# Kernel optimization log

Hardware: AMD Instinct MI355X
Metric: run time of the kernel (lower is better)

The kernel has to match this reference:

```python
import jax, jax.numpy as jnp
import numpy as np
import math

B, C, MAPS, HEADS, F, W = 2, 8, 4, 8, 256, 1024
HD = F // HEADS  # head dim = 32


def conv2d(x, w, b):
    # x [B,Ci,H,W], w [Co,Ci,3,3], SAME padding 1
    y = jax.lax.conv_general_dilated(x, w, (1, 1), [(1, 1), (1, 1)],
                                     dimension_numbers=('NCHW', 'OIHW', 'NCHW'))
    return y + b[None, :, None, None]


def mcl_feat(x, w):
    # MultichannelLinear feature transform: per-channel linear over feature dim
    # x [B,C,Fin,W], w [C,Fout,Fin] -> [B,C,Fout,W]
    return jnp.einsum('bcfw,cgf->bcgw', x, w)


def rope(x):
    # lucidrains-style rotary embedding over seq dim (-2); x [..., S, D]
    d = x.shape[-1]
    s = x.shape[-2]
    inv = 1.0 / (10000.0 ** (jnp.arange(0, d, 2, dtype=jnp.float32) / d))
    fr = jnp.arange(s, dtype=jnp.float32)[:, None] * inv[None, :]  # [S, D/2]
    cos = jnp.repeat(jnp.cos(fr), 2, axis=-1).astype(x.dtype)  # [S, D]
    sin = jnp.repeat(jnp.sin(fr), 2, axis=-1).astype(x.dtype)
    x2 = x.reshape(*x.shape[:-1], d // 2, 2)
    xr = jnp.stack((-x2[..., 1], x2[..., 0]), axis=-1).reshape(x.shape)
    return x * cos + xr * sin


def setup_inputs() -> dict:
    key = jax.random.key(0)
    ks = jax.random.split(key, 16)
    p = lambda k, shp, s=0.02: (jax.random.normal(k, shp, dtype=jnp.float32) * s)
    inp = {
        'x': jax.random.normal(ks[0], (B, C, F, W), dtype=jnp.float32),
        'prev_qk': jax.random.normal(ks[1], (B, MAPS, HEADS, W, W), dtype=jnp.float32),
        'wq_conv': p(ks[2], (MAPS, C, 3, 3)), 'bq_conv': jnp.zeros((MAPS,), jnp.float32),
        'wq_lin': p(ks[3], (MAPS, F, F)),
        'wk_conv': p(ks[4], (MAPS, C, 3, 3)), 'bk_conv': jnp.zeros((MAPS,), jnp.float32),
        'wk_lin': p(ks[5], (MAPS, F, F)),
        'wv_conv': p(ks[6], (MAPS, C, 3, 3)), 'bv_conv': jnp.zeros((MAPS,), jnp.float32),
        'wv_lin': p(ks[7], (MAPS, F, F)),
        'wo_pw': p(ks[8], (C + MAPS, F, F)),
        'wo_dw': p(ks[9], (C, C + MAPS)),
    }
    return inp


def reference(x, prev_qk, wq_conv, bq_conv, wq_lin, wk_conv, bk_conv, wk_lin,
              wv_conv, bv_conv, wv_lin, wo_pw, wo_dw):
    b, c, h, w = x.shape

    def proj(w_conv, b_conv, w_lin):
        y = mcl_feat(conv2d(x, w_conv, b_conv), w_lin)  # [B,M,F,W]
        # transpose(2,3) -> [B,M,W,F] -> split heads -> [B,M,Hd,W? ] permute
        y = y.transpose(0, 1, 3, 2).reshape(b, MAPS, w, HEADS, HD)
        return y.transpose(0, 1, 3, 2, 4)  # [B,M,Heads,W,HD]

    q = rope(proj(wq_conv, bq_conv, wq_lin))
    k = rope(proj(wk_conv, bk_conv, wk_lin))
    v = proj(wv_conv, bv_conv, wv_lin)

    # NOTE: scale is sqrt(h) = sqrt(feature/height dim), as in the original code
    qk = jnp.einsum('bmnqd,bmnkd->bmnqk', q, k) / math.sqrt(h)
    qk = qk + prev_qk
    a = jnp.einsum('bmnqk,bmnkd->bmnqd', jax.nn.softmax(qk, axis=-1), v)
    # [B,M,Heads,W,HD] -> [B,M,W,Heads*HD] -> [B,M,F,W]
    a = a.transpose(0, 1, 3, 2, 4).reshape(b, MAPS, w, -1).transpose(0, 1, 3, 2)

    cat = jnp.concatenate((x, a), axis=1)  # [B, C+M, F, W]
    out = jnp.einsum('bcfw,oc->bofw', mcl_feat(cat, wo_pw), wo_dw)  # o_proj
    return out, qk
```

## Files before the change

kernel.cpp:

```cpp
#include <hip/hip_runtime.h>
#include <hip/hip_bf16.h>
#include <stdint.h>


typedef __attribute__((ext_vector_type(8))) short s16x8;
typedef __attribute__((ext_vector_type(4))) float f32x4;

#define MFMA16(a, b, c) __builtin_amdgcn_mfma_f32_16x16x32_bf16((a), (b), (c), 0, 0, 0)

__device__ __forceinline__ short f2bf(float f) {
  unsigned u = __builtin_bit_cast(unsigned, f);
  u = (u + 0x7FFFu + ((u >> 16) & 1u)) >> 16;
  return (short)u;
}
__device__ __forceinline__ unsigned pack2(float a, float b) {
  return (unsigned)(unsigned short)f2bf(a) | ((unsigned)(unsigned short)f2bf(b) << 16);
}
__device__ __forceinline__ float bf2f(unsigned u) {
  return __builtin_bit_cast(float, u << 16);
}

__global__ __launch_bounds__(256) void k_prep(const float* wq, const float* wk,
                                              const float* wv, const float* wo,
                                              short* wlin, short* wob, float* ct, float* st) {
  int i = blockIdx.x * 256 + threadIdx.x;
  if (i < 262144) wlin[i] = f2bf(wq[i]);
  else if (i < 524288) wlin[i] = f2bf(wk[i - 262144]);
  else if (i < 786432) wlin[i] = f2bf(wv[i - 524288]);
  if (i < 786432) wob[i] = f2bf(wo[i]);
  if (i < 16384) {
    int w = i >> 4, j = i & 15;
    float inv = exp2f(-(float)j * (13.287712379549449f / 16.0f));
    float ang = (float)w * inv;
    ct[i] = cosf(ang);
    st[i] = sinf(ang);
  }
}

__device__ __forceinline__ void loadrow(float* r, const float* xc, int f, int w0) {
  if (f < 0 || f > 255) {
#pragma unroll
    for (int jj = 0; jj < 6; ++jj) r[jj] = 0.f;
    return;
  }
  const float* row = xc + f * 1024;
#pragma unroll
  for (int jj = 0; jj < 6; ++jj) {
    int wc = w0 - 1 + jj;
    r[jj] = (wc >= 0 && wc < 1024) ? row[wc] : 0.f;
  }
}

__global__ __launch_bounds__(256) void k_conv(const float* x, const float* wqc, const float* bq,
                                              const float* wkc, const float* bk,
                                              const float* wvc, const float* bv, short* y) {
  int blk = blockIdx.x;
  int m_ = blk >> 7;
  int b_ = (blk >> 6) & 1;
  int fs = blk & 63;
  int f0 = fs * 4;
  int w0 = threadIdx.x * 4;
  const float* xb = x + (size_t)b_ * 2097152;
  const float* wp_[3] = {wqc + m_ * 72, wkc + m_ * 72, wvc + m_ * 72};
  float bias_[3] = {bq[m_], bk[m_], bv[m_]};

  float acc[3][4][4];
#pragma unroll
  for (int p = 0; p < 3; ++p)
#pragma unroll
    for (int fi = 0; fi < 4; ++fi)
#pragma unroll
      for (int j = 0; j < 4; ++j) acc[p][fi][j] = bias_[p];

  for (int c = 0; c < 8; ++c) {
    const float* xc = xb + c * 262144;
    float w9[3][9];
#pragma unroll
    for (int p = 0; p < 3; ++p)
#pragma unroll
      for (int t = 0; t < 9; ++t) w9[p][t] = wp_[p][c * 9 + t];
    float rows[6][6];
#pragma unroll
    for (int ri = 0; ri < 6; ++ri) loadrow(rows[ri], xc, f0 - 1 + ri, w0);
#pragma unroll
    for (int fi = 0; fi < 4; ++fi) {
#pragma unroll
      for (int p = 0; p < 3; ++p) {
#pragma unroll
        for (int j = 0; j < 4; ++j) {
          float s = acc[p][fi][j];
          s += rows[fi][j] * w9[p][0] + rows[fi][j + 1] * w9[p][1] + rows[fi][j + 2] * w9[p][2];
          s += rows[fi + 1][j] * w9[p][3] + rows[fi + 1][j + 1] * w9[p][4] + rows[fi + 1][j + 2] * w9[p][5];
          s += rows[fi + 2][j] * w9[p][6] + rows[fi + 2][j + 1] * w9[p][7] + rows[fi + 2][j + 2] * w9[p][8];
          acc[p][fi][j] = s;
        }
      }
    }
  }
#pragma unroll
  for (int p = 0; p < 3; ++p) {
    int mat = p * 8 + b_ * 4 + m_;
    short* yp = y + (size_t)mat * 262144;
#pragma unroll
    for (int fi = 0; fi < 4; ++fi) {
      uint2 pk;
      pk.x = pack2(acc[p][fi][0], acc[p][fi][1]);
      pk.y = pack2(acc[p][fi][2], acc[p][fi][3]);
      *(uint2*)(yp + (f0 + fi) * 1024 + w0) = pk;
    }
  }
}

__global__ __launch_bounds__(256) void k_ty(const short* y, short* yT) {
  __shared__ short tile[64][66];
  int blk = blockIdx.x;
  int mat = blk >> 6;
  int t = blk & 63;
  int f0 = (t >> 4) * 64, w0 = (t & 15) * 64;
  int j = threadIdx.x & 63, i0 = threadIdx.x >> 6;
  const short* sp = y + (size_t)mat * 262144 + f0 * 1024 + w0;
#pragma unroll
  for (int k = 0; k < 16; ++k) {
    int i = i0 + k * 4;
    tile[j][i] = sp[i * 1024 + j];
  }
  __syncthreads();
  short* dp = yT + (size_t)mat * 262144 + w0 * 256 + f0;
#pragma unroll
  for (int k = 0; k < 16; ++k) {
    int i = i0 + k * 4;
    dp[i * 256 + j] = tile[i][j];
  }
}

__global__ __launch_bounds__(256) void k_tx(const float* x, short* xT) {
  __shared__ short tile[64][66];
  int blk = blockIdx.x;
  int mat = blk >> 6;
  int t = blk & 63;
  int f0 = (t >> 4) * 64, w0 = (t & 15) * 64;
  int j = threadIdx.x & 63, i0 = threadIdx.x >> 6;
  const float* sp = x + (size_t)mat * 262144 + f0 * 1024 + w0;
#pragma unroll
  for (int k = 0; k < 16; ++k) {
    int i = i0 + k * 4;
    tile[j][i] = f2bf(sp[i * 1024 + j]);
  }
  __syncthreads();
  short* dp = xT + (size_t)mat * 262144 + w0 * 256 + f0;
#pragma unroll
  for (int k = 0; k < 16; ++k) {
    int i = i0 + k * 4;
    dp[i * 256 + j] = tile[i][j];
  }
}

__global__ __launch_bounds__(256) void k_qkv(const short* wlin, const short* yT,
                                             const float* ct, const float* st,
                                             short* qws, short* kws, short* vws) {
  int blk = blockIdx.x;
  int pbm = blk >> 4, wt = blk & 15;
  int p = pbm >> 3, bm = pbm & 7;
  int m_ = bm & 3;
  int tid = threadIdx.x, wv = tid >> 6, l = tid & 63, lr = l & 15, lg = l >> 4;
  const short* wl = wlin + (p * 4 + m_) * 65536;
  const short* yp = yT + (size_t)pbm * 262144;
  int w0 = wt * 64;
  int G0 = wv * 64;
  f32x4 acc[4][4];
#pragma unroll
  for (int i = 0; i < 4; ++i)
#pragma unroll
    for (int j = 0; j < 4; ++j) acc[i][j] = (f32x4){0.f, 0.f, 0.f, 0.f};

  if (p < 2) {
    for (int kc = 0; kc < 256; kc += 32) {
      s16x8 A[4], Bf[4];
#pragma unroll
      for (int gs = 0; gs < 4; ++gs)
        A[gs] = *(const s16x8*)(wl + (G0 + gs * 16 + lr) * 256 + kc + lg * 8);
#pragma unroll
      for (int s = 0; s < 4; ++s)
        Bf[s] = *(const s16x8*)(yp + (w0 + s * 16 + lr) * 256 + kc + lg * 8);
#pragma unroll
      for (int gs = 0; gs < 4; ++gs)
#pragma unroll
        for (int s = 0; s < 4; ++s) acc[gs][s] = MFMA16(A[gs], Bf[s], acc[gs][s]);
    }
    short* dst = (p == 0) ? qws : kws;
    float scale = (p == 0) ? 0.0625f : 1.0f;
#pragma unroll
    for (int gs = 0; gs < 4; ++gs) {
      int g0v = G0 + gs * 16 + lg * 4;
      int h = g0v >> 5, d0 = g0v & 31;
      int i0 = d0 >> 1;
#pragma unroll
      for (int s = 0; s < 4; ++s) {
        int w = w0 + s * 16 + lr;
        float c0 = ct[w * 16 + i0], sn0 = st[w * 16 + i0];
        float c1 = ct[w * 16 + i0 + 1], sn1 = st[w * 16 + i0 + 1];
        f32x4 v = acc[gs][s];
        float e0 = (v[0] * c0 - v[1] * sn0) * scale;
        float e1 = (v[1] * c0 + v[0] * sn0) * scale;
        float e2 = (v[2] * c1 - v[3] * sn1) * scale;
        float e3 = (v[3] * c1 + v[2] * sn1) * scale;
        uint2 pk;
        pk.x = pack2(e0, e1);
        pk.y = pack2(e2, e3);
        *(uint2*)(dst + (((size_t)bm * 8 + h) * 1024 + w) * 32 + d0) = pk;
      }
    }
  } else {
    for (int kc = 0; kc < 256; kc += 32) {
      s16x8 A[4], Bf[4];
#pragma unroll
      for (int s = 0; s < 4; ++s)
        A[s] = *(const s16x8*)(yp + (w0 + s * 16 + lr) * 256 + kc + lg * 8);
#pragma unroll
      for (int gs = 0; gs < 4; ++gs)
        Bf[gs] = *(const s16x8*)(wl + (G0 + gs * 16 + lr) * 256 + kc + lg * 8);
#pragma unroll
      for (int s = 0; s < 4; ++s)
#pragma unroll
        for (int gs = 0; gs < 4; ++gs) acc[s][gs] = MFMA16(A[s], Bf[gs], acc[s][gs]);
    }
#pragma unroll
    for (int s = 0; s < 4; ++s) {
      int wb = w0 + s * 16 + lg * 4;
#pragma unroll
      for (int gs = 0; gs < 4; ++gs) {
        int g = G0 + gs * 16 + lr;
        f32x4 v = acc[s][gs];
        uint2 pk;
        pk.x = pack2(v[0], v[1]);
        pk.y = pack2(v[2], v[3]);
        *(uint2*)(vws + ((size_t)bm * 256 + g) * 1024 + wb) = pk;
      }
    }
  }
}

__global__ __launch_bounds__(256, 1) void k_attn(const short* qws, const short* kws,
                                                 const short* vws, const float* prev,
                                                 float* qko, short* aT) {
  __shared__ char smem[131072];
  int blk = blockIdx.x;
  int bmh = blk >> 4;
  int qg = blk & 15;
  int h = bmh & 7, bm = bmh >> 3;
  int tid = threadIdx.x;
  int wv = tid >> 6, l = tid & 63, lr = l & 15, lg = l >> 4;
  int q0 = qg * 64 + wv * 16;
  const short* qp = qws + (size_t)bmh * 32768;
  const short* kp = kws + (size_t)bmh * 32768;
  const short* vp = vws + ((size_t)bm * 256 + h * 32) * 1024;
  const float* pvb = prev + (size_t)bmh * 1048576 + (size_t)q0 * 1024;
  float* qob = qko + (size_t)bmh * 1048576 + (size_t)q0 * 1024;
  char* Sb = smem + wv * 32768;

  s16x8 qf = *(const s16x8*)(qp + (q0 + lr) * 32 + lg * 8);
  const f32x4 z4 = {0.f, 0.f, 0.f, 0.f};

#pragma unroll
  for (int w = 0; w < 16; ++w) {
    int k0 = w * 64;
    s16x8 kf[4];
#pragma unroll
    for (int s = 0; s < 4; ++s)
      kf[s] = *(const s16x8*)(kp + (k0 + s * 16 + lr) * 32 + lg * 8);
#pragma unroll
    for (int s = 0; s < 4; ++s) {
      f32x4 sx = MFMA16(kf[s], qf, z4);
      uint2 pk;
      pk.x = pack2(sx[0], sx[1]);
      pk.y = pack2(sx[2], sx[3]);
      int kb = (k0 + s * 16 + lg * 4) * 2;
      *(uint2*)(Sb + lr * 2048 + (kb ^ ((lr & 7) << 4))) = pk;
    }
  }

  float rs[16];
  f32x4 pf[3][4];
#pragma unroll
  for (int qt = 0; qt < 4; ++qt) pf[0][qt] = *(const f32x4*)(pvb + 0 * 1024 + qt * 256 + l * 4);
#pragma unroll
  for (int qt = 0; qt < 4; ++qt) pf[1][qt] = *(const f32x4*)(pvb + 1 * 1024 + qt * 256 + l * 4);
#pragma unroll
  for (int qt = 0; qt < 4; ++qt) pf[2][qt] = *(const f32x4*)(pvb + 2 * 1024 + qt * 256 + l * 4);

#pragma unroll
  for (int r = 0; r < 16; ++r) {
    float sum = 0.f;
#pragma unroll
    for (int qt = 0; qt < 4; ++qt) {
      int sb = (qt * 512 + l * 8) ^ ((r & 7) << 4);
      uint2 su = *(const uint2*)(Sb + r * 2048 + sb);
      f32x4 sv = {bf2f(su.x & 0xffffu), bf2f(su.x >> 16),
                  bf2f(su.y & 0xffffu), bf2f(su.y >> 16)};
      f32x4 v = sv + pf[r % 3][qt];
      *(f32x4*)(qob + (size_t)r * 1024 + qt * 256 + l * 4) = v;
      float e0 = __expf(v[0]), e1 = __expf(v[1]);
      float e2 = __expf(v[2]), e3 = __expf(v[3]);
      sum += (e0 + e1) + (e2 + e3);
      uint2 pk;
      pk.x = pack2(e0, e1);
      pk.y = pack2(e2, e3);
      *(uint2*)(Sb + r * 2048 + sb) = pk;
    }
    if (r + 3 < 16) {
#pragma unroll
      for (int qt = 0; qt < 4; ++qt)
        pf[r % 3][qt] = *(const f32x4*)(pvb + (size_t)(r + 3) * 1024 + qt * 256 + l * 4);
    }
    rs[r] = sum;
  }
#pragma unroll
  for (int r = 0; r < 16; ++r) {
    float s = rs[r];
    s += __shfl_xor(s, 1);
    s += __shfl_xor(s, 2);
    s += __shfl_xor(s, 4);
    s += __shfl_xor(s, 8);
    s += __shfl_xor(s, 16);
    s += __shfl_xor(s, 32);
    rs[r] = s;
  }

  f32x4 o0 = {0.f, 0.f, 0.f, 0.f}, o1 = {0.f, 0.f, 0.f, 0.f};
#pragma unroll
  for (int w = 0; w < 16; ++w) {
    int k0 = w * 64;
#pragma unroll
    for (int kc = 0; kc < 2; ++kc) {
      int kb = (k0 + kc * 32 + lg * 8) * 2;
      s16x8 pa = *(const s16x8*)(Sb + lr * 2048 + (kb ^ ((lr & 7) << 4)));
      s16x8 vf0 = *(const s16x8*)(vp + lr * 1024 + k0 + kc * 32 + lg * 8);
      o0 = MFMA16(pa, vf0, o0);
      s16x8 vf1 = *(const s16x8*)(vp + (16 + lr) * 1024 + k0 + kc * 32 + lg * 8);
      o1 = MFMA16(pa, vf1, o1);
    }
  }
#pragma unroll
  for (int j = 0; j < 4; ++j) {
    float s = (lg == 0) ? rs[j] : (lg == 1) ? rs[4 + j] : (lg == 2) ? rs[8 + j] : rs[12 + j];
    float inv = 1.0f / s;
    o0[j] *= inv;
    o1[j] *= inv;
  }
  short* ap = aT + (size_t)bm * 262144;
#pragma unroll
  for (int r = 0; r < 4; ++r) {
    int row = q0 + lg * 4 + r;
    ap[row * 256 + h * 32 + lr] = f2bf(o0[r]);
    ap[row * 256 + h * 32 + 16 + lr] = f2bf(o1[r]);
  }
}

__global__ __launch_bounds__(256) void k_zproj(const short* wopw, const short* xT,
                                               const short* aT, short* z) {
  int blk = blockIdx.x;
  int bc = blk >> 4, wt = blk & 15;
  int b_ = bc / 12, c_ = bc % 12;
  const short* src = (c_ < 8) ? (xT + ((size_t)b_ * 8 + c_) * 262144)
                              : (aT + ((size_t)b_ * 4 + (c_ - 8)) * 262144);
  const short* wl = wopw + c_ * 65536;
  int tid = threadIdx.x, wv = tid >> 6, l = tid & 63, lr = l & 15, lg = l >> 4;
  int w0 = wt * 64, G0 = wv * 64;
  f32x4 acc[4][4];
#pragma unroll
  for (int i = 0; i < 4; ++i)
#pragma unroll
    for (int j = 0; j < 4; ++j) acc[i][j] = (f32x4){0.f, 0.f, 0.f, 0.f};
  for (int kc = 0; kc < 256; kc += 32) {
    s16x8 A[4], Bf[4];
#pragma unroll
    for (int s = 0; s < 4; ++s)
      A[s] = *(const s16x8*)(src + (w0 + s * 16 + lr) * 256 + kc + lg * 8);
#pragma unroll
    for (int gs = 0; gs < 4; ++gs)
      Bf[gs] = *(const s16x8*)(wl + (G0 + gs * 16 + lr) * 256 + kc + lg * 8);
#pragma unroll
    for (int s = 0; s < 4; ++s)
#pragma unroll
      for (int gs = 0; gs < 4; ++gs) acc[s][gs] = MFMA16(A[s], Bf[gs], acc[s][gs]);
  }
  short* zp = z + (size_t)bc * 262144;
#pragma unroll
  for (int s = 0; s < 4; ++s) {
    int wb = w0 + s * 16 + lg * 4;
#pragma unroll
    for (int gs = 0; gs < 4; ++gs) {
      int g = G0 + gs * 16 + lr;
      f32x4 v = acc[s][gs];
      uint2 pk;
      pk.x = pack2(v[0], v[1]);
      pk.y = pack2(v[2], v[3]);
      *(uint2*)(zp + g * 1024 + wb) = pk;
    }
  }
}

__global__ __launch_bounds__(256) void k_dw(const short* z, const float* dw, float* out0) {
  __shared__ float wdw[96];
  if (threadIdx.x < 96) wdw[threadIdx.x] = dw[threadIdx.x];
  __syncthreads();
  int id = blockIdx.x * 256 + threadIdx.x;
  int w4 = id & 255, g = (id >> 8) & 255, b_ = id >> 16;
  const short* zb = z + ((size_t)b_ * 12) * 262144 + g * 1024 + w4 * 4;
  float zv[12][4];
#pragma unroll
  for (int c = 0; c < 12; ++c) {
    uint2 u = *(const uint2*)(zb + (size_t)c * 262144);
    zv[c][0] = bf2f(u.x & 0xffffu);
    zv[c][1] = bf2f(u.x >> 16);
    zv[c][2] = bf2f(u.y & 0xffffu);
    zv[c][3] = bf2f(u.y >> 16);
  }
  float* ob = out0 + ((size_t)b_ * 8) * 262144 + g * 1024 + w4 * 4;
#pragma unroll
  for (int o = 0; o < 8; ++o) {
    f32x4 s = {0.f, 0.f, 0.f, 0.f};
#pragma unroll
    for (int c = 0; c < 12; ++c) {
      float wc = wdw[o * 12 + c];
      s[0] += wc * zv[c][0];
      s[1] += wc * zv[c][1];
      s[2] += wc * zv[c][2];
      s[3] += wc * zv[c][3];
    }
    __builtin_nontemporal_store(s, (f32x4*)(ob + (size_t)o * 262144));
  }
}

extern "C" void kernel_launch(void* const* d_in, const int* in_sizes, int n_in,
                              void* d_out, int out_size, void* d_ws, size_t ws_size,
                              hipStream_t stream) {
  const float* x = (const float*)d_in[0];
  const float* prevqk = (const float*)d_in[1];
  const float* wq_conv = (const float*)d_in[2];
  const float* bq = (const float*)d_in[3];
  const float* wq_lin = (const float*)d_in[4];
  const float* wk_conv = (const float*)d_in[5];
  const float* bk = (const float*)d_in[6];
  const float* wk_lin = (const float*)d_in[7];
  const float* wv_conv = (const float*)d_in[8];
  const float* bv = (const float*)d_in[9];
  const float* wv_lin = (const float*)d_in[10];
  const float* wo_pw = (const float*)d_in[11];
  const float* wo_dw = (const float*)d_in[12];

  float* out0 = (float*)d_out;
  float* qkout = out0 + 4194304;

  char* ws = (char*)d_ws;
  short* wlin_b = (short*)ws;
  short* wopw_b = wlin_b + 786432;
  float* ct = (float*)(ws + 3145728);
  float* st = ct + 16384;
  short* y_b = (short*)(ws + 3276800);
  short* yT_b = y_b + 6291456;
  short* q_b = yT_b + 6291456;
  short* k_b = q_b + 2097152;
  short* v_b = k_b + 2097152;
  short* xT_b = v_b + 2097152;
  short* aT_b = xT_b + 4194304;
  short* z_b = (short*)(ws + 53608448);

  k_prep<<<3072, 256, 0, stream>>>(wq_lin, wk_lin, wv_lin, wo_pw, wlin_b, wopw_b, ct, st);
  k_conv<<<512, 256, 0, stream>>>(x, wq_conv, bq, wk_conv, bk, wv_conv, bv, y_b);
  k_ty<<<1536, 256, 0, stream>>>(y_b, yT_b);
  k_tx<<<1024, 256, 0, stream>>>(x, xT_b);
  k_qkv<<<384, 256, 0, stream>>>(wlin_b, yT_b, ct, st, q_b, k_b, v_b);
  k_attn<<<1024, 256, 0, stream>>>(q_b, k_b, v_b, prevqk, qkout, aT_b);
  k_zproj<<<384, 256, 0, stream>>>(wopw_b, xT_b, aT_b, z_b);
  k_dw<<<512, 256, 0, stream>>>(z_b, wo_dw, out0);
}
```

Before: 253.2 us.

## Merge prep, conv and x-transpose kernels; batch prev_qk loads with nontemporal stores

Three independent preprocessing kernels (weight bf16 conversion plus rope tables, the 3x3 conv, and the x transpose) are folded into one launch that dispatches on block index, removing two launches and letting their blocks run concurrently. In the attention softmax stage, prev_qk loads are restructured into double-buffered groups of four rows. The qk output is written with nontemporal stores before the exp pass. This raises register pressure in the attention kernel and puts heterogeneous blocks in one grid with a shared-memory tile that only some blocks use.

```diff
diff --git a/kernel.cpp b/kernel.cpp
--- a/kernel.cpp
+++ b/kernel.cpp
@@ -20,23 +20,6 @@
   return __builtin_bit_cast(float, u << 16);
 }
 
-__global__ __launch_bounds__(256) void k_prep(const float* wq, const float* wk,
-                                              const float* wv, const float* wo,
-                                              short* wlin, short* wob, float* ct, float* st) {
-  int i = blockIdx.x * 256 + threadIdx.x;
-  if (i < 262144) wlin[i] = f2bf(wq[i]);
-  else if (i < 524288) wlin[i] = f2bf(wk[i - 262144]);
-  else if (i < 786432) wlin[i] = f2bf(wv[i - 524288]);
-  if (i < 786432) wob[i] = f2bf(wo[i]);
-  if (i < 16384) {
-    int w = i >> 4, j = i & 15;
-    float inv = exp2f(-(float)j * (13.287712379549449f / 16.0f));
-    float ang = (float)w * inv;
-    ct[i] = cosf(ang);
-    st[i] = sinf(ang);
-  }
-}
-
 __device__ __forceinline__ void loadrow(float* r, const float* xc, int f, int w0) {
   if (f < 0 || f > 255) {
 #pragma unroll
@@ -51,62 +34,111 @@
   }
 }
 
-__global__ __launch_bounds__(256) void k_conv(const float* x, const float* wqc, const float* bq,
-                                              const float* wkc, const float* bk,
-                                              const float* wvc, const float* bv, short* y) {
-  int blk = blockIdx.x;
-  int m_ = blk >> 7;
-  int b_ = (blk >> 6) & 1;
-  int fs = blk & 63;
-  int f0 = fs * 4;
-  int w0 = threadIdx.x * 4;
-  const float* xb = x + (size_t)b_ * 2097152;
-  const float* wp_[3] = {wqc + m_ * 72, wkc + m_ * 72, wvc + m_ * 72};
-  float bias_[3] = {bq[m_], bk[m_], bv[m_]};
-
-  float acc[3][4][4];
-#pragma unroll
-  for (int p = 0; p < 3; ++p)
-#pragma unroll
-    for (int fi = 0; fi < 4; ++fi)
-#pragma unroll
-      for (int j = 0; j < 4; ++j) acc[p][fi][j] = bias_[p];
-
-  for (int c = 0; c < 8; ++c) {
-    const float* xc = xb + c * 262144;
-    float w9[3][9];
+__global__ __launch_bounds__(256) void k_pre(const float* x,
+                                             const float* wq, const float* wk,
+                                             const float* wv, const float* wo,
+                                             const float* wqc, const float* bq,
+                                             const float* wkc, const float* bk,
+                                             const float* wvc, const float* bv,
+                                             short* wlin, short* wob, float* ct, float* st,
+                                             short* y, short* xT) {
+  __shared__ short tile[64][66];
+  int B = blockIdx.x;
+  int tid = threadIdx.x;
+
+  if (B < 3072) {
+    int i = B * 256 + tid;
+    if (i < 262144) wlin[i] = f2bf(wq[i]);
+    else if (i < 524288) wlin[i] = f2bf(wk[i - 262144]);
+    else if (i < 786432) wlin[i] = f2bf(wv[i - 524288]);
+    if (i < 786432) wob[i] = f2bf(wo[i]);
+    if (i < 16384) {
+      int w = i >> 4, j = i & 15;
+      float inv = exp2f(-(float)j * (13.287712379549449f / 16.0f));
+      float ang = (float)w * inv;
+      ct[i] = cosf(ang);
+      st[i] = sinf(ang);
+    }
+    return;
+  }
+
+  if (B < 3584) {
+    int blk = B - 3072;
+    int m_ = blk >> 7;
+    int b_ = (blk >> 6) & 1;
+    int fs = blk & 63;
+    int f0 = fs * 4;
+    int w0 = tid * 4;
+    const float* xb = x + (size_t)b_ * 2097152;
+    const float* wp_[3] = {wqc + m_ * 72, wkc + m_ * 72, wvc + m_ * 72};
+    float bias_[3] = {bq[m_], bk[m_], bv[m_]};
+
+    float acc[3][4][4];
 #pragma unroll
     for (int p = 0; p < 3; ++p)
 #pragma unroll
-      for (int t = 0; t < 9; ++t) w9[p][t] = wp_[p][c * 9 + t];
-    float rows[6][6];
-#pragma unroll
-    for (int ri = 0; ri < 6; ++ri) loadrow(rows[ri], xc, f0 - 1 + ri, w0);
-#pragma unroll
-    for (int fi = 0; fi < 4; ++fi) {
-#pragma unroll
-      for (int p = 0; p < 3; ++p) {
-#pragma unroll
-        for (int j = 0; j < 4; ++j) {
-          float s = acc[p][fi][j];
-          s += rows[fi][j] * w9[p][0] + rows[fi][j + 1] * w9[p][1] + rows[fi][j + 2] * w9[p][2];
-          s += rows[fi + 1][j] * w9[p][3] + rows[fi + 1][j + 1] * w9[p][4] + rows[fi + 1][j + 2] * w9[p][5];
-          s += rows[fi + 2][j] * w9[p][6] + rows[fi + 2][j + 1] * w9[p][7] + rows[fi + 2][j + 2] * w9[p][8];
-          acc[p][fi][j] = s;
+      for (int fi = 0; fi < 4; ++fi)
+#pragma unroll
+        for (int j = 0; j < 4; ++j) acc[p][fi][j] = bias_[p];
+
+    for (int c = 0; c < 8; ++c) {
+      const float* xc = xb + c * 262144;
+      float w9[3][9];
+#pragma unroll
+      for (int p = 0; p < 3; ++p)
+#pragma unroll
+        for (int t = 0; t < 9; ++t) w9[p][t] = wp_[p][c * 9 + t];
+      float rows[6][6];
+#pragma unroll
+      for (int ri = 0; ri < 6; ++ri) loadrow(rows[ri], xc, f0 - 1 + ri, w0);
+#pragma unroll
+      for (int fi = 0; fi < 4; ++fi) {
+#pragma unroll
+        for (int p = 0; p < 3; ++p) {
+#pragma unroll
+          for (int j = 0; j < 4; ++j) {
+            float s = acc[p][fi][j];
+            s += rows[fi][j] * w9[p][0] + rows[fi][j + 1] * w9[p][1] + rows[fi][j + 2] * w9[p][2];
+            s += rows[fi + 1][j] * w9[p][3] + rows[fi + 1][j + 1] * w9[p][4] + rows[fi + 1][j + 2] * w9[p][5];
+            s += rows[fi + 2][j] * w9[p][6] + rows[fi + 2][j + 1] * w9[p][7] + rows[fi + 2][j + 2] * w9[p][8];
+            acc[p][fi][j] = s;
+          }
         }
       }
     }
-  }
-#pragma unroll
-  for (int p = 0; p < 3; ++p) {
-    int mat = p * 8 + b_ * 4 + m_;
-    short* yp = y + (size_t)mat * 262144;
-#pragma unroll
-    for (int fi = 0; fi < 4; ++fi) {
-      uint2 pk;
-      pk.x = pack2(acc[p][fi][0], acc[p][fi][1]);
-      pk.y = pack2(acc[p][fi][2], acc[p][fi][3]);
-      *(uint2*)(yp + (f0 + fi) * 1024 + w0) = pk;
+#pragma unroll
+    for (int p = 0; p < 3; ++p) {
+      int mat = p * 8 + b_ * 4 + m_;
+      short* yp = y + (size_t)mat * 262144;
+#pragma unroll
+      for (int fi = 0; fi < 4; ++fi) {
+        uint2 pk;
+        pk.x = pack2(acc[p][fi][0], acc[p][fi][1]);
+        pk.y = pack2(acc[p][fi][2], acc[p][fi][3]);
+        *(uint2*)(yp + (f0 + fi) * 1024 + w0) = pk;
+      }
+    }
+    return;
+  }
+
+  {
+    int blk = B - 3584;
+    int mat = blk >> 6;
+    int t = blk & 63;
+    int f0 = (t >> 4) * 64, w0 = (t & 15) * 64;
+    int j = tid & 63, i0 = tid >> 6;
+    const float* sp = x + (size_t)mat * 262144 + f0 * 1024 + w0;
+#pragma unroll
+    for (int k = 0; k < 16; ++k) {
+      int i = i0 + k * 4;
+      tile[j][i] = f2bf(sp[i * 1024 + j]);
+    }
+    __syncthreads();
+    short* dp = xT + (size_t)mat * 262144 + w0 * 256 + f0;
+#pragma unroll
+    for (int k = 0; k < 16; ++k) {
+      int i = i0 + k * 4;
+      dp[i * 256 + j] = tile[i][j];
     }
   }
 }
@@ -126,28 +158,6 @@
   }
   __syncthreads();
   short* dp = yT + (size_t)mat * 262144 + w0 * 256 + f0;
-#pragma unroll
-  for (int k = 0; k < 16; ++k) {
-    int i = i0 + k * 4;
-    dp[i * 256 + j] = tile[i][j];
-  }
-}
-
-__global__ __launch_bounds__(256) void k_tx(const float* x, short* xT) {
-  __shared__ short tile[64][66];
-  int blk = blockIdx.x;
-  int mat = blk >> 6;
-  int t = blk & 63;
-  int f0 = (t >> 4) * 64, w0 = (t & 15) * 64;
-  int j = threadIdx.x & 63, i0 = threadIdx.x >> 6;
-  const float* sp = x + (size_t)mat * 262144 + f0 * 1024 + w0;
-#pragma unroll
-  for (int k = 0; k < 16; ++k) {
-    int i = i0 + k * 4;
-    tile[j][i] = f2bf(sp[i * 1024 + j]);
-  }
-  __syncthreads();
-  short* dp = xT + (size_t)mat * 262144 + w0 * 256 + f0;
 #pragma unroll
   for (int k = 0; k < 16; ++k) {
     int i = i0 + k * 4;
@@ -280,39 +290,65 @@
   }
 
   float rs[16];
-  f32x4 pf[3][4];
-#pragma unroll
-  for (int qt = 0; qt < 4; ++qt) pf[0][qt] = *(const f32x4*)(pvb + 0 * 1024 + qt * 256 + l * 4);
-#pragma unroll
-  for (int qt = 0; qt < 4; ++qt) pf[1][qt] = *(const f32x4*)(pvb + 1 * 1024 + qt * 256 + l * 4);
-#pragma unroll
-  for (int qt = 0; qt < 4; ++qt) pf[2][qt] = *(const f32x4*)(pvb + 2 * 1024 + qt * 256 + l * 4);
-
-#pragma unroll
-  for (int r = 0; r < 16; ++r) {
-    float sum = 0.f;
-#pragma unroll
-    for (int qt = 0; qt < 4; ++qt) {
-      int sb = (qt * 512 + l * 8) ^ ((r & 7) << 4);
-      uint2 su = *(const uint2*)(Sb + r * 2048 + sb);
-      f32x4 sv = {bf2f(su.x & 0xffffu), bf2f(su.x >> 16),
-                  bf2f(su.y & 0xffffu), bf2f(su.y >> 16)};
-      f32x4 v = sv + pf[r % 3][qt];
-      *(f32x4*)(qob + (size_t)r * 1024 + qt * 256 + l * 4) = v;
-      float e0 = __expf(v[0]), e1 = __expf(v[1]);
-      float e2 = __expf(v[2]), e3 = __expf(v[3]);
-      sum += (e0 + e1) + (e2 + e3);
-      uint2 pk;
-      pk.x = pack2(e0, e1);
-      pk.y = pack2(e2, e3);
-      *(uint2*)(Sb + r * 2048 + sb) = pk;
-    }
-    if (r + 3 < 16) {
+  f32x4 pA[4][4], pB[4][4];
+#pragma unroll
+  for (int r4 = 0; r4 < 4; ++r4)
+#pragma unroll
+    for (int qt = 0; qt < 4; ++qt)
+      pA[r4][qt] = *(const f32x4*)(pvb + (size_t)r4 * 1024 + qt * 256 + l * 4);
+#pragma unroll
+  for (int r4 = 0; r4 < 4; ++r4)
+#pragma unroll
+    for (int qt = 0; qt < 4; ++qt)
+      pB[r4][qt] = *(const f32x4*)(pvb + (size_t)(4 + r4) * 1024 + qt * 256 + l * 4);
+
+#pragma unroll
+  for (int g = 0; g < 4; ++g) {
+    f32x4(&cur)[4][4] = (g & 1) ? pB : pA;
+    f32x4 v[4][4];
+#pragma unroll
+    for (int r4 = 0; r4 < 4; ++r4) {
+      int r = g * 4 + r4;
+#pragma unroll
+      for (int qt = 0; qt < 4; ++qt) {
+        int sb = (qt * 512 + l * 8) ^ ((r & 7) << 4);
+        uint2 su = *(const uint2*)(Sb + r * 2048 + sb);
+        f32x4 sv = {bf2f(su.x & 0xffffu), bf2f(su.x >> 16),
+                    bf2f(su.y & 0xffffu), bf2f(su.y >> 16)};
+        v[r4][qt] = sv + cur[r4][qt];
+      }
+    }
+#pragma unroll
+    for (int r4 = 0; r4 < 4; ++r4)
 #pragma unroll
       for (int qt = 0; qt < 4; ++qt)
-        pf[r % 3][qt] = *(const f32x4*)(pvb + (size_t)(r + 3) * 1024 + qt * 256 + l * 4);
-    }
-    rs[r] = sum;
+        __builtin_nontemporal_store(v[r4][qt],
+            (f32x4*)(qob + (size_t)(g * 4 + r4) * 1024 + qt * 256 + l * 4));
+    if (g < 2) {
+#pragma unroll
+      for (int r4 = 0; r4 < 4; ++r4)
+#pragma unroll
+        for (int qt = 0; qt < 4; ++qt)
+          cur[r4][qt] = *(const f32x4*)(pvb + (size_t)((g + 2) * 4 + r4) * 1024 + qt * 256 + l * 4);
+    }
+#pragma unroll
+    for (int r4 = 0; r4 < 4; ++r4) {
+      int r = g * 4 + r4;
+      float sum = 0.f;
+#pragma unroll
+      for (int qt = 0; qt < 4; ++qt) {
+        f32x4 w_ = v[r4][qt];
+        float e0 = __expf(w_[0]), e1 = __expf(w_[1]);
+        float e2 = __expf(w_[2]), e3 = __expf(w_[3]);
+        sum += (e0 + e1) + (e2 + e3);
+        uint2 pk;
+        pk.x = pack2(e0, e1);
+        pk.y = pack2(e2, e3);
+        int sb = (qt * 512 + l * 8) ^ ((r & 7) << 4);
+        *(uint2*)(Sb + r * 2048 + sb) = pk;
+      }
+      rs[r] = sum;
+    }
   }
 #pragma unroll
   for (int r = 0; r < 16; ++r) {
@@ -466,10 +502,10 @@
   short* aT_b = xT_b + 4194304;
   short* z_b = (short*)(ws + 53608448);
 
-  k_prep<<<3072, 256, 0, stream>>>(wq_lin, wk_lin, wv_lin, wo_pw, wlin_b, wopw_b, ct, st);
-  k_conv<<<512, 256, 0, stream>>>(x, wq_conv, bq, wk_conv, bk, wv_conv, bv, y_b);
+  k_pre<<<4608, 256, 0, stream>>>(x, wq_lin, wk_lin, wv_lin, wo_pw,
+                                  wq_conv, bq, wk_conv, bk, wv_conv, bv,
+                                  wlin_b, wopw_b, ct, st, y_b, xT_b);
   k_ty<<<1536, 256, 0, stream>>>(y_b, yT_b);
-  k_tx<<<1024, 256, 0, stream>>>(x, xT_b);
   k_qkv<<<384, 256, 0, stream>>>(wlin_b, yT_b, ct, st, q_b, k_b, v_b);
   k_attn<<<1024, 256, 0, stream>>>(q_b, k_b, v_b, prevqk, qkout, aT_b);
   k_zproj<<<384, 256, 0, stream>>>(wopw_b, xT_b, aT_b, z_b);
```

After: 255.0 us. No clear change (+0.7%).
